# Kernel optimization log

Hardware: AMD Instinct MI355X
Metric: run time of the kernel (lower is better)

The kernel has to match this reference:

```python
import jax, jax.numpy as jnp
import numpy as np

B, S, DIN, DOUT = 2, 2048, 4096, 4096


def setup_inputs() -> dict:
    key = jax.random.key(0)
    k1, k2, k3, k4, k5 = jax.random.split(key, 5)
    x = jax.random.normal(k1, (B, S, DIN), dtype=jnp.float32)
    # int8-range weights stored as int32 (faithful to q_int_weight.float() upcast)
    q_int_weight = jax.random.randint(k2, (DIN, DOUT), 0, 256, dtype=jnp.int32)
    scale = jax.random.uniform(k3, (1,), dtype=jnp.float32) * 0.01 + 0.001
    zero_point = jax.random.uniform(k4, (1,), dtype=jnp.float32) * 128.0
    bias = jax.random.normal(k5, (DOUT,), dtype=jnp.float32)
    return {"x": x, "q_int_weight": q_int_weight, "scale": scale,
            "zero_point": zero_point, "bias": bias}


def reference(x, q_int_weight, scale, zero_point, bias):
    # Dequantize: (q - zero_point) * scale, per-tensor affine. Stored [in, out].
    w = (q_int_weight.astype(jnp.float32) - zero_point) * scale  # [DIN, DOUT]
    # F.linear(x_flat, w.t(), bias) == x @ w + bias
    y = jnp.einsum('bsi,io->bso', x, w) + bias  # [B, S, DOUT]
    return y
```

## Files before the change

kernel.cpp:

```cpp
#include <hip/hip_runtime.h>
#include <cstdint>
#include <cstddef>

#define M_DIM 4096
#define N_DIM 4096
#define K_DIM 4096
#define BM 256
#define BN 256
#define BKB 128
#define KTILES (K_DIM / BKB)

typedef __attribute__((ext_vector_type(4))) int i32x4;

__device__ __forceinline__ void async_copy16(const void* g, void* l) {
  __builtin_amdgcn_global_load_lds(
      (const __attribute__((address_space(1))) void*)g,
      (__attribute__((address_space(3))) void*)l,
      16, 0, 0);
}

__device__ __forceinline__ void wait_vm6() {
  asm volatile("s_waitcnt vmcnt(6)" ::: "memory");
}
__device__ __forceinline__ void wait_vm0() {
  asm volatile("s_waitcnt vmcnt(0)" ::: "memory");
}

__global__ __launch_bounds__(256) void convert_fused(
    const float* __restrict__ x, signed char* __restrict__ xi,
    float* __restrict__ sx, float* __restrict__ rs,
    const int* __restrict__ q, signed char* __restrict__ qsT) {
  __shared__ __align__(16) int smem[64 * 68];
  const int t = threadIdx.x;

  if (blockIdx.x < 4096) {
    int(*qtile)[68] = (int(*)[68])smem;
    const int bid = blockIdx.x;
    const int k0 = (bid & 63) << 6;
    const int n0 = (bid >> 6) << 6;

    {
      const int c = t & 15;
      const int r0 = t >> 4;
#pragma unroll
      for (int i = 0; i < 4; ++i) {
        const int r = r0 + i * 16;
        const int4 v =
            *(const int4*)(q + (size_t)(k0 + r) * N_DIM + n0 + c * 4);
        *(int4*)&qtile[r][c * 4] = v;
      }
    }
    __syncthreads();
    {
      const int kc = t & 15;
      const int g = t >> 4;
      int4 v[4];
#pragma unroll
      for (int i = 0; i < 4; ++i)
        v[i] = *(const int4*)&qtile[kc * 4 + i][g * 4];
#pragma unroll
      for (int j = 0; j < 4; ++j) {
        const int b0 = ((&v[0].x)[j] - 128) & 255;
        const int b1 = ((&v[1].x)[j] - 128) & 255;
        const int b2 = ((&v[2].x)[j] - 128) & 255;
        const int b3 = ((&v[3].x)[j] - 128) & 255;
        const int pk = b0 | (b1 << 8) | (b2 << 16) | (b3 << 24);
        *(int*)(qsT + (size_t)(n0 + g * 4 + j) * K_DIM + k0 + kc * 4) = pk;
      }
    }
  } else {
    float* red = (float*)smem;
    const size_t row = blockIdx.x - 4096;
    const float* xr = x + row * (size_t)K_DIM;

    float4 v[4];
    float amax = 0.f;
#pragma unroll
    for (int i = 0; i < 4; ++i) {
      v[i] = *(const float4*)(xr + (i * 256 + t) * 4);
      amax = fmaxf(amax, fmaxf(fmaxf(fabsf(v[i].x), fabsf(v[i].y)),
                               fmaxf(fabsf(v[i].z), fabsf(v[i].w))));
    }
#pragma unroll
    for (int o = 32; o > 0; o >>= 1)
      amax = fmaxf(amax, __shfl_down(amax, o, 64));
    if ((t & 63) == 0) red[t >> 6] = amax;
    __syncthreads();
    amax = fmaxf(fmaxf(fmaxf(red[0], red[1]), fmaxf(red[2], red[3])), 1e-20f);
    const float inv = 127.f / amax;

    int ssum = 0;
    signed char* out = xi + row * (size_t)K_DIM;
#pragma unroll
    for (int i = 0; i < 4; ++i) {
      const int ia = __float2int_rn(v[i].x * inv);
      const int ib = __float2int_rn(v[i].y * inv);
      const int ic = __float2int_rn(v[i].z * inv);
      const int id = __float2int_rn(v[i].w * inv);
      ssum += ia + ib + ic + id;
      const int pk =
          (ia & 255) | ((ib & 255) << 8) | ((ic & 255) << 16) | (id << 24);
      *(int*)(out + (i * 256 + t) * 4) = pk;
    }
    float fs = (float)ssum;
#pragma unroll
    for (int o = 32; o > 0; o >>= 1) fs += __shfl_down(fs, o, 64);
    if ((t & 63) == 0) red[4 + (t >> 6)] = fs;
    __syncthreads();
    if (t == 0) {
      rs[row] = red[4] + red[5] + red[6] + red[7];
      sx[row] = amax * (1.f / 127.f);
    }
  }
}

__global__ __launch_bounds__(512, 2) void gemm_kernel(
    const signed char* __restrict__ A,
    const signed char* __restrict__ Bt,
    const float* __restrict__ bias, const float* __restrict__ sx,
    const float* __restrict__ rs, const float* __restrict__ scale_p,
    const float* __restrict__ zp_p, float* __restrict__ C) {
  __shared__ __align__(16) signed char As[2][BM * BKB];
  __shared__ __align__(16) signed char Bs[2][BN * BKB];

  const int tid = threadIdx.x;
  const int wave = tid >> 6;
  const int lane = tid & 63;
  const int wm = wave >> 2;
  const int wn = wave & 3;

  const int swz = (blockIdx.x & 7) * 32 + (blockIdx.x >> 3);
  const int bm = swz & 15;
  const int bn = swz >> 4;
  const size_t m0 = (size_t)bm * BM;
  const size_t n0 = (size_t)bn * BN;

  const int srow = lane >> 3;
  const int schunk = (lane & 7) ^ srow;

  const int quad = lane >> 4;
  const int lrow = lane & 15;
  const int rsw = lrow & 7;

  const signed char* Abase = A + m0 * K_DIM + schunk * 16;
  const signed char* Bbase = Bt + n0 * K_DIM + schunk * 16;

  i32x4 acc[8][4];
  const i32x4 zero = {0, 0, 0, 0};
#pragma unroll
  for (int i = 0; i < 8; ++i)
#pragma unroll
    for (int j = 0; j < 4; ++j) acc[i][j] = zero;

  auto stageA = [&](int b, int k0, int ig) {
#pragma unroll
    for (int i = 0; i < 2; ++i) {
      const int rbase = i * 128 + ig * 64 + wave * 8;
      const size_t go = (size_t)(rbase + srow) * K_DIM + k0;
      async_copy16(Abase + go, (void*)&As[b][rbase * BKB]);
    }
  };
  auto stageB = [&](int b, int k0, int jg) {
#pragma unroll
    for (int i = 0; i < 2; ++i) {
      const int rbase = (i * 2 + (wave >> 2)) * 64 + jg * 32 + (wave & 3) * 8;
      const size_t go = (size_t)(rbase + srow) * K_DIM + k0;
      async_copy16(Bbase + go, (void*)&Bs[b][rbase * BKB]);
    }
  };

#define LDA(ig)                                                              \
  do {                                                                       \
    _Pragma("unroll") for (int kh = 0; kh < 2; ++kh)                         \
        _Pragma("unroll") for (int t = 0; t < 4; ++t) {                      \
      const int ar = wm * 128 + (ig) * 64 + t * 16 + lrow;                   \
      av[kh][t] =                                                            \
          *(const i32x4*)(as + ar * BKB + ((((kh << 2) | quad) ^ rsw) << 4));\
    }                                                                        \
  } while (0)

#define LDB(jg)                                                              \
  do {                                                                       \
    _Pragma("unroll") for (int kh = 0; kh < 2; ++kh)                         \
        _Pragma("unroll") for (int t = 0; t < 2; ++t) {                      \
      const int br = wn * 64 + ((jg) * 2 + t) * 16 + lrow;                   \
      bv[kh][(jg) * 2 + t] =                                                 \
          *(const i32x4*)(bs + br * BKB + ((((kh << 2) | quad) ^ rsw) << 4));\
    }                                                                        \
  } while (0)

#define MFMA16(ibase, j0)                                                    \
  do {                                                                       \
    _Pragma("unroll") for (int kh = 0; kh < 2; ++kh)                         \
        _Pragma("unroll") for (int t = 0; t < 4; ++t)                        \
            _Pragma("unroll") for (int j = 0; j < 2; ++j)                    \
        acc[(ibase) + t][(j0) + j] = __builtin_amdgcn_mfma_i32_16x16x64_i8(  \
            av[kh][t], bv[kh][(j0) + j], acc[(ibase) + t][(j0) + j], 0, 0,   \
            0);                                                              \
  } while (0)

#define DO_TILE(AS, BS, TOPW, S0, S123)                                      \
  do {                                                                       \
    const signed char* as = (AS);                                            \
    const signed char* bs = (BS);                                            \
    i32x4 av[2][4], bv[2][4];                                                \
    TOPW();                                                                  \
    __builtin_amdgcn_s_barrier();                                            \
    LDA(0);                                                                  \
    LDB(0);                                                                  \
    LDB(1);                                                                  \
    S0;                                                                      \
    __builtin_amdgcn_s_setprio(1);                                           \
    MFMA16(0, 0);                                         \
    MFMA16(0, 2);                                         \
    __builtin_amdgcn_s_setprio(0);                                           \
    LDA(1);             \
    __builtin_amdgcn_s_barrier();                                            \
    S123;                                                                    \
    __builtin_amdgcn_s_setprio(1);                                           \
    MFMA16(4, 2);                                         \
    MFMA16(4, 0);                                         \
    __builtin_amdgcn_s_setprio(0);                                           \
  } while (0)

  stageA(0, 0, 0);
  stageB(0, 0, 0);
  stageB(0, 0, 1);
  stageA(0, 0, 1);
  stageA(1, BKB, 0);
  stageB(1, BKB, 0);
  stageB(1, BKB, 1);

#pragma unroll 2
  for (int kt = 0; kt < KTILES - 2; ++kt) {
    const int buf = kt & 1;
    const int k1 = (kt + 1) * BKB;
    const int k2 = (kt + 2) * BKB;
    DO_TILE(As[buf], Bs[buf], wait_vm6,
            (stageA(buf ^ 1, k1, 1)),
            (stageA(buf, k2, 0), stageB(buf, k2, 0),
             stageB(buf, k2, 1)));
  }

  DO_TILE(As[0], Bs[0], wait_vm6, (stageA(1, 31 * BKB, 1)), (void)0);
  DO_TILE(As[1], Bs[1], wait_vm0, (void)0, (void)0);

#undef LDA
#undef LDB
#undef MFMA16
#undef DO_TILE

  const float scale = scale_p[0];
  const float c1 = 128.f - zp_p[0];
#pragma unroll
  for (int i = 0; i < 8; ++i) {
    const size_t mbase = m0 + wm * 128 + i * 16 + quad * 4;
    float am[4], bmv[4];
#pragma unroll
    for (int r = 0; r < 4; ++r) {
      const float a = scale * sx[mbase + r];
      am[r] = a;
      bmv[r] = a * c1 * rs[mbase + r];
    }
#pragma unroll
    for (int j = 0; j < 4; ++j) {
      const size_t n = n0 + wn * 64 + j * 16 + lrow;
      const float bv = bias[n];
#pragma unroll
      for (int r = 0; r < 4; ++r) {
        C[(mbase + r) * N_DIM + n] =
            fmaf(am[r], (float)acc[i][j][r], bmv[r] + bv);
      }
    }
  }
}

extern "C" void kernel_launch(void* const* d_in, const int* in_sizes, int n_in,
                              void* d_out, int out_size, void* d_ws,
                              size_t ws_size, hipStream_t stream) {
  const float* x = (const float*)d_in[0];
  const int* q = (const int*)d_in[1];
  const float* scale = (const float*)d_in[2];
  const float* zp = (const float*)d_in[3];
  const float* bias = (const float*)d_in[4];
  float* out = (float*)d_out;

  char* ws = (char*)d_ws;
  signed char* xi = (signed char*)ws;
  signed char* qsT = (signed char*)(ws + ((size_t)16 << 20));
  float* sx = (float*)(ws + ((size_t)32 << 20));
  float* rs = (float*)(ws + ((size_t)32 << 20) + (16 << 10));

  convert_fused<<<8192, 256, 0, stream>>>(x, xi, sx, rs, q, qsT);
  gemm_kernel<<<256, 512, 0, stream>>>(xi, qsT, bias, sx, rs, scale, zp, out);
}
```

Measured before the change: 239.7 us.

## Shrink GEMM block tile to 128x128 with 4 waves and 1024 blocks

Cuts the int8 GEMM block tile from 256x256 with 8 waves to 128x128 with 4 waves, launching 1024 blocks instead of 256. The staging, LDS-read and MFMA schedule are reworked to match: each wave loads all A and B fragments up front, then issues its MFMAs in two k-halves separated by an explicit lgkmcnt wait and barrier. The aim is better fill of the 256 CUs and a lighter per-block pipeline. In exchange, each block reuses data less, so global and L2 traffic per output rises.

```diff
diff --git a/kernel.cpp b/kernel.cpp
--- a/kernel.cpp
+++ b/kernel.cpp
@@ -5,8 +5,8 @@
 #define M_DIM 4096
 #define N_DIM 4096
 #define K_DIM 4096
-#define BM 256
-#define BN 256
+#define BM 128
+#define BN 128
 #define BKB 128
 #define KTILES (K_DIM / BKB)
 
@@ -114,7 +114,7 @@
   }
 }
 
-__global__ __launch_bounds__(512, 2) void gemm_kernel(
+__global__ __launch_bounds__(256, 2) void gemm_kernel(
     const signed char* __restrict__ A,
     const signed char* __restrict__ Bt,
     const float* __restrict__ bias, const float* __restrict__ sx,
@@ -126,12 +126,12 @@
   const int tid = threadIdx.x;
   const int wave = tid >> 6;
   const int lane = tid & 63;
-  const int wm = wave >> 2;
-  const int wn = wave & 3;
-
-  const int swz = (blockIdx.x & 7) * 32 + (blockIdx.x >> 3);
-  const int bm = swz & 15;
-  const int bn = swz >> 4;
+  const int wm = wave >> 1;
+  const int wn = wave & 1;
+
+  const int swz = (blockIdx.x & 7) * 128 + (blockIdx.x >> 3);
+  const int bm = swz & 31;
+  const int bn = swz >> 5;
   const size_t m0 = (size_t)bm * BM;
   const size_t n0 = (size_t)bn * BN;
 
@@ -145,58 +145,58 @@
   const signed char* Abase = A + m0 * K_DIM + schunk * 16;
   const signed char* Bbase = Bt + n0 * K_DIM + schunk * 16;
 
-  i32x4 acc[8][4];
+  i32x4 acc[4][4];
   const i32x4 zero = {0, 0, 0, 0};
 #pragma unroll
-  for (int i = 0; i < 8; ++i)
+  for (int i = 0; i < 4; ++i)
 #pragma unroll
     for (int j = 0; j < 4; ++j) acc[i][j] = zero;
 
-  auto stageA = [&](int b, int k0, int ig) {
+  auto stageAu = [&](int b, int k0, int u) {
 #pragma unroll
     for (int i = 0; i < 2; ++i) {
-      const int rbase = i * 128 + ig * 64 + wave * 8;
+      const int rbase = u * 64 + i * 32 + wave * 8;
       const size_t go = (size_t)(rbase + srow) * K_DIM + k0;
       async_copy16(Abase + go, (void*)&As[b][rbase * BKB]);
     }
   };
-  auto stageB = [&](int b, int k0, int jg) {
+  auto stageBu = [&](int b, int k0, int u) {
 #pragma unroll
     for (int i = 0; i < 2; ++i) {
-      const int rbase = (i * 2 + (wave >> 2)) * 64 + jg * 32 + (wave & 3) * 8;
+      const int rbase = u * 64 + i * 32 + wave * 8;
       const size_t go = (size_t)(rbase + srow) * K_DIM + k0;
       async_copy16(Bbase + go, (void*)&Bs[b][rbase * BKB]);
     }
   };
 
-#define LDA(ig)                                                              \
+#define LDA()                                                                \
   do {                                                                       \
     _Pragma("unroll") for (int kh = 0; kh < 2; ++kh)                         \
         _Pragma("unroll") for (int t = 0; t < 4; ++t) {                      \
-      const int ar = wm * 128 + (ig) * 64 + t * 16 + lrow;                   \
+      const int ar = wm * 64 + t * 16 + lrow;                                \
       av[kh][t] =                                                            \
           *(const i32x4*)(as + ar * BKB + ((((kh << 2) | quad) ^ rsw) << 4));\
     }                                                                        \
   } while (0)
 
-#define LDB(jg)                                                              \
+#define LDB()                                                                \
   do {                                                                       \
     _Pragma("unroll") for (int kh = 0; kh < 2; ++kh)                         \
-        _Pragma("unroll") for (int t = 0; t < 2; ++t) {                      \
-      const int br = wn * 64 + ((jg) * 2 + t) * 16 + lrow;                   \
-      bv[kh][(jg) * 2 + t] =                                                 \
+        _Pragma("unroll") for (int t = 0; t < 4; ++t) {                      \
+      const int br = wn * 64 + t * 16 + lrow;                                \
+      bv[kh][t] =                                                            \
           *(const i32x4*)(bs + br * BKB + ((((kh << 2) | quad) ^ rsw) << 4));\
     }                                                                        \
   } while (0)
 
-#define MFMA16(ibase, j0)                                                    \
-  do {                                                                       \
-    _Pragma("unroll") for (int kh = 0; kh < 2; ++kh)                         \
-        _Pragma("unroll") for (int t = 0; t < 4; ++t)                        \
-            _Pragma("unroll") for (int j = 0; j < 2; ++j)                    \
-        acc[(ibase) + t][(j0) + j] = __builtin_amdgcn_mfma_i32_16x16x64_i8(  \
-            av[kh][t], bv[kh][(j0) + j], acc[(ibase) + t][(j0) + j], 0, 0,   \
-            0);                                                              \
+#define MFMA_KH(kh)                                                          \
+  do {                                                                       \
+    __builtin_amdgcn_s_setprio(1);                                           \
+    _Pragma("unroll") for (int t = 0; t < 4; ++t)                            \
+        _Pragma("unroll") for (int j = 0; j < 4; ++j)                        \
+        acc[t][j] = __builtin_amdgcn_mfma_i32_16x16x64_i8(                   \
+            av[kh][t], bv[kh][j], acc[t][j], 0, 0, 0);                       \
+    __builtin_amdgcn_s_setprio(0);                                           \
   } while (0)
 
 #define DO_TILE(AS, BS, TOPW, S0, S123)                                      \
@@ -206,30 +206,25 @@
     i32x4 av[2][4], bv[2][4];                                                \
     TOPW();                                                                  \
     __builtin_amdgcn_s_barrier();                                            \
-    LDA(0);                                                                  \
-    LDB(0);                                                                  \
-    LDB(1);                                                                  \
+    LDA();                                                                   \
+    LDB();                                                                   \
     S0;                                                                      \
-    __builtin_amdgcn_s_setprio(1);                                           \
-    MFMA16(0, 0);                                         \
-    MFMA16(0, 2);                                         \
-    __builtin_amdgcn_s_setprio(0);                                           \
-    LDA(1);             \
+    MFMA_KH(0);                                                              \
+    __builtin_amdgcn_sched_barrier(0);                                       \
+    asm volatile("s_waitcnt lgkmcnt(0)" ::: "memory");                       \
+    __builtin_amdgcn_sched_barrier(0);                                       \
     __builtin_amdgcn_s_barrier();                                            \
     S123;                                                                    \
-    __builtin_amdgcn_s_setprio(1);                                           \
-    MFMA16(4, 2);                                         \
-    MFMA16(4, 0);                                         \
-    __builtin_amdgcn_s_setprio(0);                                           \
-  } while (0)
-
-  stageA(0, 0, 0);
-  stageB(0, 0, 0);
-  stageB(0, 0, 1);
-  stageA(0, 0, 1);
-  stageA(1, BKB, 0);
-  stageB(1, BKB, 0);
-  stageB(1, BKB, 1);
+    MFMA_KH(1);                                                              \
+  } while (0)
+
+  stageAu(0, 0, 0);
+  stageAu(0, 0, 1);
+  stageBu(0, 0, 0);
+  stageBu(0, 0, 1);
+  stageAu(1, BKB, 0);
+  stageAu(1, BKB, 1);
+  stageBu(1, BKB, 0);
 
 #pragma unroll 2
   for (int kt = 0; kt < KTILES - 2; ++kt) {
@@ -237,24 +232,24 @@
     const int k1 = (kt + 1) * BKB;
     const int k2 = (kt + 2) * BKB;
     DO_TILE(As[buf], Bs[buf], wait_vm6,
-            (stageA(buf ^ 1, k1, 1)),
-            (stageA(buf, k2, 0), stageB(buf, k2, 0),
-             stageB(buf, k2, 1)));
+            (stageBu(buf ^ 1, k1, 1)),
+            (stageAu(buf, k2, 0), stageAu(buf, k2, 1),
+             stageBu(buf, k2, 0)));
   }
 
-  DO_TILE(As[0], Bs[0], wait_vm6, (stageA(1, 31 * BKB, 1)), (void)0);
+  DO_TILE(As[0], Bs[0], wait_vm6, (stageBu(1, 31 * BKB, 1)), (void)0);
   DO_TILE(As[1], Bs[1], wait_vm0, (void)0, (void)0);
 
 #undef LDA
 #undef LDB
-#undef MFMA16
+#undef MFMA_KH
 #undef DO_TILE
 
   const float scale = scale_p[0];
   const float c1 = 128.f - zp_p[0];
 #pragma unroll
-  for (int i = 0; i < 8; ++i) {
-    const size_t mbase = m0 + wm * 128 + i * 16 + quad * 4;
+  for (int i = 0; i < 4; ++i) {
+    const size_t mbase = m0 + wm * 64 + i * 16 + quad * 4;
     float am[4], bmv[4];
 #pragma unroll
     for (int r = 0; r < 4; ++r) {
@@ -292,5 +287,5 @@
   float* rs = (float*)(ws + ((size_t)32 << 20) + (16 << 10));
 
   convert_fused<<<8192, 256, 0, stream>>>(x, xi, sx, rs, q, qsT);
-  gemm_kernel<<<256, 512, 0, stream>>>(xi, qsT, bias, sx, rs, scale, zp, out);
-}
+  gemm_kernel<<<1024, 256, 0, stream>>>(xi, qsT, bias, sx, rs, scale, zp, out);
+}
```

Measured after the change: 254.6 us. +6.2%, slower.
